# Performance work log

Measured on AMD Instinct MI355X. Metric: run time of the kernel, lower is better.

The kernel has to match this reference:

```python
import jax, jax.numpy as jnp
import numpy as np

B, C_IN, C_MID, C_OUT, R, K = 2048, 64, 64, 128, 60, 13
EPS = 1e-5


def _gather(x, nei):
    # x: [B, C, 60] -> gather neighbors -> [B, C, 60, 13]
    b, c = x.shape[0], x.shape[1]
    return x[:, :, nei].reshape(b, c, R, K)


def _block(x, nei, g, bta, m, v, W, c):
    # BN (eval mode) -> ReLU -> Conv2d(kernel (1,13)) fused block.
    h = _gather(x, nei)                              # [B,C,60,13]
    inv = g * jax.lax.rsqrt(v + EPS)                 # [C]
    h = jax.nn.relu(h * inv[None, :, None, None] + (bta - m * inv)[None, :, None, None])
    # Conv2d with kernel (1,13), stride 1 == contraction over (c, k)
    return jnp.einsum('bcrk,ock->bor', h, W) + c[None, :, None]  # [B,O,60]


def setup_inputs() -> dict:
    key = jax.random.key(0)
    ks = jax.random.split(key, 24)
    n = lambda k, s: jax.random.normal(k, s, dtype=jnp.float32)
    u = lambda k, s: jax.random.uniform(k, s, dtype=jnp.float32, minval=0.5, maxval=1.5)
    return {
        "x": n(ks[0], (B, C_IN, R)),
        "nei": jax.random.randint(ks[1], (R * K,), 0, R, dtype=jnp.int32),
        # comb_layer_in: BN(in) + Conv(in->mid)
        "g1": n(ks[2], (C_IN,)), "b1": n(ks[3], (C_IN,)), "m1": n(ks[4], (C_IN,)), "v1": u(ks[5], (C_IN,)),
        "W1": n(ks[6], (C_MID, C_IN, K)) * 0.1, "c1": n(ks[7], (C_MID,)) * 0.1,
        # comb_layer_out: BN(mid) + Conv(mid->out)
        "g2": n(ks[8], (C_MID,)), "b2": n(ks[9], (C_MID,)), "m2": n(ks[10], (C_MID,)), "v2": u(ks[11], (C_MID,)),
        "W2": n(ks[12], (C_OUT, C_MID, K)) * 0.1, "c2": n(ks[13], (C_OUT,)) * 0.1,
        # short_cut_layer: BN(in) + Conv(in->out)
        "g3": n(ks[14], (C_IN,)), "b3": n(ks[15], (C_IN,)), "m3": n(ks[16], (C_IN,)), "v3": u(ks[17], (C_IN,)),
        "W3": n(ks[18], (C_OUT, C_IN, K)) * 0.1, "c3": n(ks[19], (C_OUT,)) * 0.1,
    }


def reference(x, nei, g1, b1, m1, v1, W1, c1, g2, b2, m2, v2, W2, c2,
              g3, b3, m3, v3, W3, c3):
    f = _block(x, nei, g1, b1, m1, v1, W1, c1)      # [B, C_MID, 60]
    f = _block(f, nei, g2, b2, m2, v2, W2, c2)      # [B, C_OUT, 60]
    sc = _block(x, nei, g3, b3, m3, v3, W3, c3)     # [B, C_OUT, 60]
    return f + sc
```

## Files before the change

kernel.cpp:

```cpp
#include <hip/hip_runtime.h>
#include <hip/hip_bf16.h>


typedef __attribute__((ext_vector_type(8))) short bf16x8;
typedef __attribute__((ext_vector_type(4))) float f32x4;
typedef __attribute__((ext_vector_type(4))) unsigned short us4;
typedef __attribute__((ext_vector_type(8))) unsigned short us8;

#define EPSV 1e-5f
#define PLANE 131072
#define ZTOT  7864320

__device__ __forceinline__ unsigned short f2bf(float f) {
  unsigned int u = __builtin_bit_cast(unsigned int, f);
  u += 0x7FFFu + ((u >> 16) & 1u);
  return (unsigned short)(u >> 16);
}
__device__ __forceinline__ float bf2f(unsigned short s) {
  unsigned int u = ((unsigned int)s) << 16;
  return __builtin_bit_cast(float, u);
}

typedef const __attribute__((address_space(1))) unsigned int gas_u32;
typedef __attribute__((address_space(3))) unsigned int las_u32;
__device__ __forceinline__ void gl16(const void* g, void* l) {
  __builtin_amdgcn_global_load_lds((gas_u32*)g, (las_u32*)l, 16, 0, 0);
}

__global__ void prep_w(const float* __restrict__ W1, const float* __restrict__ W2,
                       const float* __restrict__ W3,
                       const float* __restrict__ g1, const float* __restrict__ be1,
                       const float* __restrict__ mu1, const float* __restrict__ va1,
                       const float* __restrict__ c1,
                       const float* __restrict__ g2, const float* __restrict__ be2,
                       const float* __restrict__ mu2, const float* __restrict__ va2,
                       const float* __restrict__ c2,
                       const float* __restrict__ g3, const float* __restrict__ be3,
                       const float* __restrict__ mu3, const float* __restrict__ va3,
                       const float* __restrict__ c3,
                       unsigned short* __restrict__ W1t,
                       unsigned short* __restrict__ W23t,
                       float* __restrict__ params) {
  int t = blockIdx.x * 256 + threadIdx.x;
  if (t < 4096) {
    int o = t >> 6, c = t & 63;
    const float* src = W1 + (o * 64 + c) * 13;
    unsigned short* dst = W1t + o * 832 + c;
    #pragma unroll
    for (int ks = 0; ks < 13; ks++) dst[ks * 64] = f2bf(src[ks]);
  } else if (t < 20480) {
    int idx = t - 4096;
    int half = idx >> 13;
    int o = (idx >> 6) & 127, c = idx & 63;
    const float* src = (half ? W3 : W2) + (o * 64 + c) * 13;
    unsigned short* dst = W23t + o * 1664 + half * 13 * 64 + c;
    #pragma unroll
    for (int ks = 0; ks < 13; ks++) dst[ks * 64] = f2bf(src[ks]);
  }
  if (blockIdx.x == 79) {
    int u = threadIdx.x;
    if (u < 64) {
      float a1v = g1[u] * rsqrtf(va1[u] + EPSV);
      params[u]       = a1v;
      params[64 + u]  = be1[u] - mu1[u] * a1v;
      float a3v = g3[u] * rsqrtf(va3[u] + EPSV);
      params[128 + u] = a3v;
      params[192 + u] = be3[u] - mu3[u] * a3v;
      float a2v = g2[u] * rsqrtf(va2[u] + EPSV);
      params[256 + u] = a2v;
      params[320 + u] = be2[u] - mu2[u] * a2v + a2v * c1[u];
    }
    if (u < 128) params[384 + u] = c2[u] + c3[u];
  }
}

__global__ __launch_bounds__(256) void t_in(const float* __restrict__ x,
                                            const float* __restrict__ params,
                                            unsigned short* __restrict__ z1T,
                                            unsigned short* __restrict__ z3T) {
  __shared__ float xt[64 * 61];
  __shared__ float prm[256];
  const int b = blockIdx.x, t = threadIdx.x;
  prm[t] = params[t];
  for (int i = t; i < 3840; i += 256) {
    int c = i / 60;
    xt[c * 61 + (i - c * 60)] = x[b * 3840 + i];
  }
  __syncthreads();
  if (t < 240) {
    int r = t >> 2, g = t & 3, c0 = g << 4;
    us8 z1v0, z1v1, z3v0, z3v1;
    #pragma unroll
    for (int j = 0; j < 8; j++) {
      int c = c0 + j;
      float v = xt[c * 61 + r];
      z1v0[j] = f2bf(fmaxf(fmaf(v, prm[c], prm[64 + c]), 0.f));
      z3v0[j] = f2bf(fmaxf(fmaf(v, prm[128 + c], prm[192 + c]), 0.f));
    }
    #pragma unroll
    for (int j = 0; j < 8; j++) {
      int c = c0 + 8 + j;
      float v = xt[c * 61 + r];
      z1v1[j] = f2bf(fmaxf(fmaf(v, prm[c], prm[64 + c]), 0.f));
      z3v1[j] = f2bf(fmaxf(fmaf(v, prm[128 + c], prm[192 + c]), 0.f));
    }
    int idx = (r * 2048 + b) * 64 + c0;
    *(us8*)(z1T + idx) = z1v0;  *(us8*)(z1T + idx + 8) = z1v1;
    *(us8*)(z3T + idx) = z3v0;  *(us8*)(z3T + idx + 8) = z3v1;
  }
}

#define MFMA __builtin_amdgcn_mfma_f32_16x16x32_bf16

__global__ __launch_bounds__(256, 2) void gemm1(const unsigned short* __restrict__ W1t,
                                                const unsigned short* __restrict__ z1T,
                                                const int* __restrict__ nei,
                                                const float* __restrict__ params,
                                                unsigned short* __restrict__ z2T) {
  __shared__ unsigned short As[2][4096];
  __shared__ unsigned short Bs[2][2][8192];

  const int bid = blockIdx.x;
  const int rp = bid >> 4, btile = bid & 15;
  const int b0 = btile << 7;
  const int rA = rp * 2, rB = rA + 1;
  const int t = threadIdx.x, wave = t >> 6, lane = t & 63;
  const int quad = lane >> 4, nl = lane & 15;
  const int rsel = wave >> 1, nhh = wave & 1;

  int pl0[13], pl1[13];
  #pragma unroll
  for (int q = 0; q < 13; q++) { pl0[q] = nei[rA * 13 + q]; pl1[q] = nei[rB * 13 + q]; }

  const int trow = t >> 3, tj = t & 7;
  const int sw8 = ((tj ^ (trow & 7)) << 3);
  const unsigned short* gA = W1t + trow * 832 + tj * 8;
  const unsigned short* gB = z1T + (b0 + trow) * 64 + tj * 8;
  unsigned short* lA = &As[0][trow * 64 + sw8];
  unsigned short* lB0 = &Bs[0][0][trow * 64 + sw8];
  unsigned short* lB1 = &Bs[0][1][trow * 64 + sw8];

  {
    us8 va0 = *(const us8*)(gA);
    us8 va1 = *(const us8*)(gA + 32 * 832);
    const unsigned short* g0 = gB + pl0[0] * PLANE;
    const unsigned short* g1p = gB + pl1[0] * PLANE;
    us8 b00 = *(const us8*)(g0);
    us8 b01 = *(const us8*)(g0 + 2048);
    us8 b02 = *(const us8*)(g0 + 4096);
    us8 b03 = *(const us8*)(g0 + 6144);
    us8 b10 = *(const us8*)(g1p);
    us8 b11 = *(const us8*)(g1p + 2048);
    us8 b12 = *(const us8*)(g1p + 4096);
    us8 b13 = *(const us8*)(g1p + 6144);
    *(us8*)(lA) = va0;  *(us8*)(lA + 2048) = va1;
    *(us8*)(lB0) = b00; *(us8*)(lB0 + 2048) = b01;
    *(us8*)(lB0 + 4096) = b02; *(us8*)(lB0 + 6144) = b03;
    *(us8*)(lB1) = b10; *(us8*)(lB1 + 2048) = b11;
    *(us8*)(lB1 + 4096) = b12; *(us8*)(lB1 + 6144) = b13;
  }
  __syncthreads();

  const int c0 = ((quad ^ (nl & 7)) << 3);
  f32x4 acc[4][4] = {};
  #pragma unroll 1
  for (int kq = 0; kq < 13; kq++) {
    const int bf = kq & 1;
    us8 va0, va1, b00, b01, b02, b03, b10, b11, b12, b13;
    if (kq < 12) {
      const unsigned short* ga = gA + (kq + 1) * 64;
      va0 = *(const us8*)(ga);
      va1 = *(const us8*)(ga + 32 * 832);
      const unsigned short* g0 = gB + pl0[kq + 1] * PLANE;
      const unsigned short* g1p = gB + pl1[kq + 1] * PLANE;
      b00 = *(const us8*)(g0);        b01 = *(const us8*)(g0 + 2048);
      b02 = *(const us8*)(g0 + 4096); b03 = *(const us8*)(g0 + 6144);
      b10 = *(const us8*)(g1p);        b11 = *(const us8*)(g1p + 2048);
      b12 = *(const us8*)(g1p + 4096); b13 = *(const us8*)(g1p + 6144);
    }
    const unsigned short* Ab = &As[bf][nl * 64];
    const unsigned short* Bb = &Bs[bf][rsel][(nhh * 64 + nl) * 64];
    bf16x8 af[4][2], bfr[4][2];
    #pragma unroll
    for (int mt = 0; mt < 4; mt++) {
      af[mt][0] = *(const bf16x8*)(Ab + mt * 1024 + c0);
      af[mt][1] = *(const bf16x8*)(Ab + mt * 1024 + (c0 ^ 32));
    }
    #pragma unroll
    for (int nt = 0; nt < 4; nt++) {
      bfr[nt][0] = *(const bf16x8*)(Bb + nt * 1024 + c0);
      bfr[nt][1] = *(const bf16x8*)(Bb + nt * 1024 + (c0 ^ 32));
    }
    #pragma unroll
    for (int h = 0; h < 2; h++)
      #pragma unroll
      for (int mt = 0; mt < 4; mt++)
        #pragma unroll
        for (int nt = 0; nt < 4; nt++)
          acc[mt][nt] = MFMA(af[mt][h], bfr[nt][h], acc[mt][nt], 0, 0, 0);
    if (kq < 12) {
      unsigned short* la = lA + (bf ^ 1) * 4096;
      unsigned short* l0 = lB0 + (bf ^ 1) * 16384;
      unsigned short* l1 = lB1 + (bf ^ 1) * 16384;
      *(us8*)(la) = va0;  *(us8*)(la + 2048) = va1;
      *(us8*)(l0) = b00; *(us8*)(l0 + 2048) = b01;
      *(us8*)(l0 + 4096) = b02; *(us8*)(l0 + 6144) = b03;
      *(us8*)(l1) = b10; *(us8*)(l1 + 2048) = b11;
      *(us8*)(l1 + 4096) = b12; *(us8*)(l1 + 6144) = b13;
    }
    __syncthreads();
  }

  const int rr = rA + rsel;
  #pragma unroll
  for (int mt = 0; mt < 4; mt++) {
    int ob = mt * 16 + quad * 4;
    f32x4 av = *(const f32x4*)(params + 256 + ob);
    f32x4 bv = *(const f32x4*)(params + 320 + ob);
    #pragma unroll
    for (int nt = 0; nt < 4; nt++) {
      int col = b0 + nhh * 64 + nt * 16 + nl;
      f32x4 a = acc[mt][nt];
      us4 w;
      w.x = f2bf(fmaxf(fmaf(a[0], av[0], bv[0]), 0.f));
      w.y = f2bf(fmaxf(fmaf(a[1], av[1], bv[1]), 0.f));
      w.z = f2bf(fmaxf(fmaf(a[2], av[2], bv[2]), 0.f));
      w.w = f2bf(fmaxf(fmaf(a[3], av[3], bv[3]), 0.f));
      *(us4*)(z2T + (rr * 2048 + col) * 64 + ob) = w;
    }
  }
}

__global__ __launch_bounds__(256, 2) void gemm2(const unsigned short* __restrict__ W23t,
                                                const unsigned short* __restrict__ z2T,
                                                const unsigned short* __restrict__ z3T,
                                                const int* __restrict__ nei,
                                                const float* __restrict__ params,
                                                unsigned short* __restrict__ outT) {
  __shared__ unsigned short As[2][4096];
  __shared__ unsigned short Bs[2][8192];

  const int bid = blockIdx.x;
  const int r = bid >> 3, btile = bid & 7;
  const int b0 = btile << 8;
  const int t = threadIdx.x, wv = t >> 6, lane = t & 63;
  const int quad = lane >> 4, nl = lane & 15;
  const int mh = wv >> 1, nh = wv & 1;

  const int neibase = r * 13;

  const int lr = lane >> 2, lj = lane & 3;
  int aoff[2];
  #pragma unroll
  for (int i = 0; i < 2; i++) aoff[i] = (16 * (2 * wv + i) + lr) * 3328 + lj * 16;
  int boff[4];
  #pragma unroll
  for (int i = 0; i < 4; i++) boff[i] = (b0 + 16 * (4 * wv + i) + lr) * 128 + lj * 16;

  const char* gAb = (const char*)W23t;

  {
    int p0 = nei[neibase];
    const char* gb = (const char*)(z2T + p0 * PLANE);
    #pragma unroll
    for (int i = 0; i < 2; i++)
      gl16(gAb + aoff[i], &As[0][(2 * wv + i) * 512]);
    #pragma unroll
    for (int i = 0; i < 4; i++)
      gl16(gb + boff[i], &Bs[0][(4 * wv + i) * 512]);
  }
  asm volatile("s_waitcnt vmcnt(0)" ::: "memory");
  __syncthreads();

  f32x4 acc[4][8] = {};
  #pragma unroll 1
  for (int s = 0; s < 52; s++) {
    const int buf = s & 1;
    if (s < 51) {
      const int kn = s + 1;
      const int pn = kn >> 1, hn = kn & 1;
      int p = nei[neibase + (pn < 13 ? pn : pn - 13)];
      const char* ga = gAb + pn * 128 + hn * 64;
      const char* gb = (const char*)((pn < 13 ? z2T : z3T) + p * PLANE) + hn * 64;
      #pragma unroll
      for (int i = 0; i < 2; i++)
        gl16(ga + aoff[i], &As[buf ^ 1][(2 * wv + i) * 512]);
      #pragma unroll
      for (int i = 0; i < 4; i++)
        gl16(gb + boff[i], &Bs[buf ^ 1][(4 * wv + i) * 512]);
    }
    const unsigned short* Ab = &As[buf][(mh * 64 + nl) * 32 + quad * 8];
    const unsigned short* Bb = &Bs[buf][(nh * 128 + nl) * 32 + quad * 8];
    bf16x8 af[4], bfr[8];
    #pragma unroll
    for (int mt = 0; mt < 4; mt++)
      af[mt] = *(const bf16x8*)(Ab + mt * 512);
    #pragma unroll
    for (int nt = 0; nt < 8; nt++)
      bfr[nt] = *(const bf16x8*)(Bb + nt * 512);
    #pragma unroll
    for (int mt = 0; mt < 4; mt++)
      #pragma unroll
      for (int nt = 0; nt < 8; nt++)
        acc[mt][nt] = MFMA(af[mt], bfr[nt], acc[mt][nt], 0, 0, 0);
    asm volatile("s_waitcnt vmcnt(0)" ::: "memory");
    __syncthreads();
  }

  #pragma unroll
  for (int mt = 0; mt < 4; mt++) {
    int ob = mh * 64 + mt * 16 + quad * 4;
    f32x4 cv = *(const f32x4*)(params + 384 + ob);
    #pragma unroll
    for (int nt = 0; nt < 8; nt++) {
      int col = b0 + nh * 128 + nt * 16 + nl;
      f32x4 a = acc[mt][nt];
      us4 w;
      w.x = f2bf(a[0] + cv[0]);
      w.y = f2bf(a[1] + cv[1]);
      w.z = f2bf(a[2] + cv[2]);
      w.w = f2bf(a[3] + cv[3]);
      *(us4*)(outT + (r * 2048 + col) * 128 + ob) = w;
    }
  }
}

__global__ __launch_bounds__(256) void t_out(const unsigned short* __restrict__ outT,
                                             float* __restrict__ out) {
  __shared__ float ot[60 * 129];
  const int b = blockIdx.x, t = threadIdx.x;
  for (int i = t; i < 1920; i += 256) {
    int r = i >> 5, og = (i & 31) << 2;
    us4 v = *(const us4*)(outT + (r * 2048 + b) * 128 + og);
    ot[r * 129 + og + 0] = bf2f(v.x);
    ot[r * 129 + og + 1] = bf2f(v.y);
    ot[r * 129 + og + 2] = bf2f(v.z);
    ot[r * 129 + og + 3] = bf2f(v.w);
  }
  __syncthreads();
  int o = t >> 1, s = t & 1;
  float* dst = out + b * 7680 + o * 60 + s * 30;
  #pragma unroll
  for (int j = 0; j < 30; j++) dst[j] = ot[(s * 30 + j) * 129 + o];
}

extern "C" void kernel_launch(void* const* d_in, const int* in_sizes, int n_in,
                              void* d_out, int out_size, void* d_ws, size_t ws_size,
                              hipStream_t stream) {
  const float* x   = (const float*)d_in[0];
  const int*   nei = (const int*)d_in[1];
  const float* g1  = (const float*)d_in[2];
  const float* be1 = (const float*)d_in[3];
  const float* mu1 = (const float*)d_in[4];
  const float* va1 = (const float*)d_in[5];
  const float* W1  = (const float*)d_in[6];
  const float* c1  = (const float*)d_in[7];
  const float* g2  = (const float*)d_in[8];
  const float* be2 = (const float*)d_in[9];
  const float* mu2 = (const float*)d_in[10];
  const float* va2 = (const float*)d_in[11];
  const float* W2  = (const float*)d_in[12];
  const float* c2  = (const float*)d_in[13];
  const float* g3  = (const float*)d_in[14];
  const float* be3 = (const float*)d_in[15];
  const float* mu3 = (const float*)d_in[16];
  const float* va3 = (const float*)d_in[17];
  const float* W3  = (const float*)d_in[18];
  const float* c3  = (const float*)d_in[19];

  unsigned short* W1t  = (unsigned short*)d_ws;
  unsigned short* W23t = W1t + 53248;
  float*          prm  = (float*)(W23t + 212992);
  unsigned short* z2T  = (unsigned short*)(prm + 512);
  unsigned short* z3T  = z2T + ZTOT;
  unsigned short* big  = z3T + ZTOT;
  unsigned short* z1T  = big;
  unsigned short* outT = big;

  prep_w<<<80, 256, 0, stream>>>(W1, W2, W3,
                                 g1, be1, mu1, va1, c1,
                                 g2, be2, mu2, va2, c2,
                                 g3, be3, mu3, va3, c3,
                                 W1t, W23t, prm);
  t_in<<<2048, 256, 0, stream>>>(x, prm, z1T, z3T);
  gemm1<<<480, 256, 0, stream>>>(W1t, z1T, nei, prm, z2T);
  gemm2<<<480, 256, 0, stream>>>(W23t, z2T, z3T, nei, prm, outT);
  t_out<<<2048, 256, 0, stream>>>(outT, (float*)d_out);
}
```

Baseline: 245.0 us.

## Triple-buffer gemm2 LDS loads with swizzled layout and precomputed neighbor offsets

```diff
diff --git a/kernel.cpp b/kernel.cpp
--- a/kernel.cpp
+++ b/kernel.cpp
@@ -237,8 +237,9 @@
                                                 const int* __restrict__ nei,
                                                 const float* __restrict__ params,
                                                 unsigned short* __restrict__ outT) {
-  __shared__ unsigned short As[2][4096];
-  __shared__ unsigned short Bs[2][8192];
+  __shared__ unsigned short As[3][4096];
+  __shared__ unsigned short Bs[3][8192];
+  __shared__ int sOff[26];
 
   const int bid = blockIdx.x;
   const int r = bid >> 3, btile = bid & 7;
@@ -247,50 +248,62 @@
   const int quad = lane >> 4, nl = lane & 15;
   const int mh = wv >> 1, nh = wv & 1;
 
-  const int neibase = r * 13;
+  if (t < 26) {
+    int idx = t < 13 ? t : t - 13;
+    int p = nei[r * 13 + idx];
+    sOff[t] = p * (PLANE * 2) + (t < 13 ? 0 : ZTOT * 2);
+  }
 
   const int lr = lane >> 2, lj = lane & 3;
+  const int sj = ((lj ^ ((lr >> 1) & 3)) << 4);
   int aoff[2];
   #pragma unroll
-  for (int i = 0; i < 2; i++) aoff[i] = (16 * (2 * wv + i) + lr) * 3328 + lj * 16;
+  for (int i = 0; i < 2; i++) aoff[i] = (16 * (2 * wv + i) + lr) * 3328 + sj;
   int boff[4];
   #pragma unroll
-  for (int i = 0; i < 4; i++) boff[i] = (b0 + 16 * (4 * wv + i) + lr) * 128 + lj * 16;
+  for (int i = 0; i < 4; i++) boff[i] = (b0 + 16 * (4 * wv + i) + lr) * 128 + sj;
 
   const char* gAb = (const char*)W23t;
+  const char* z2b = (const char*)z2T;
+
+  __syncthreads();
 
   {
-    int p0 = nei[neibase];
-    const char* gb = (const char*)(z2T + p0 * PLANE);
-    #pragma unroll
-    for (int i = 0; i < 2; i++)
-      gl16(gAb + aoff[i], &As[0][(2 * wv + i) * 512]);
-    #pragma unroll
-    for (int i = 0; i < 4; i++)
-      gl16(gb + boff[i], &Bs[0][(4 * wv + i) * 512]);
-  }
-  asm volatile("s_waitcnt vmcnt(0)" ::: "memory");
-  __syncthreads();
+    const char* gb = z2b + sOff[0];
+    #pragma unroll
+    for (int i = 0; i < 2; i++) gl16(gAb + aoff[i], &As[0][(2 * wv + i) * 512]);
+    #pragma unroll
+    for (int i = 0; i < 4; i++) gl16(gb + boff[i], &Bs[0][(4 * wv + i) * 512]);
+    #pragma unroll
+    for (int i = 0; i < 2; i++) gl16(gAb + 64 + aoff[i], &As[1][(2 * wv + i) * 512]);
+    #pragma unroll
+    for (int i = 0; i < 4; i++) gl16(gb + 64 + boff[i], &Bs[1][(4 * wv + i) * 512]);
+  }
+
+  const int rc = ((quad ^ ((nl >> 1) & 3)) << 3);
+  const int aro = (mh * 64 + nl) * 32 + rc;
+  const int bro = (nh * 128 + nl) * 32 + rc;
 
   f32x4 acc[4][8] = {};
+  int cb = 0, sb = 2;
   #pragma unroll 1
-  for (int s = 0; s < 52; s++) {
-    const int buf = s & 1;
-    if (s < 51) {
-      const int kn = s + 1;
-      const int pn = kn >> 1, hn = kn & 1;
-      int p = nei[neibase + (pn < 13 ? pn : pn - 13)];
-      const char* ga = gAb + pn * 128 + hn * 64;
-      const char* gb = (const char*)((pn < 13 ? z2T : z3T) + p * PLANE) + hn * 64;
+  for (int s = 0; s < 51; s++) {
+    asm volatile("s_waitcnt vmcnt(6)" ::: "memory");
+    __builtin_amdgcn_s_barrier();
+    __builtin_amdgcn_sched_barrier(0);
+    const int kn = s + 2;
+    if (kn < 52) {
+      const int pn = kn >> 1;
+      int off = sOff[pn] + ((kn & 1) << 6);
+      const char* ga = gAb + kn * 64;
+      const char* gb = z2b + off;
       #pragma unroll
-      for (int i = 0; i < 2; i++)
-        gl16(ga + aoff[i], &As[buf ^ 1][(2 * wv + i) * 512]);
+      for (int i = 0; i < 2; i++) gl16(ga + aoff[i], &As[sb][(2 * wv + i) * 512]);
       #pragma unroll
-      for (int i = 0; i < 4; i++)
-        gl16(gb + boff[i], &Bs[buf ^ 1][(4 * wv + i) * 512]);
-    }
-    const unsigned short* Ab = &As[buf][(mh * 64 + nl) * 32 + quad * 8];
-    const unsigned short* Bb = &Bs[buf][(nh * 128 + nl) * 32 + quad * 8];
+      for (int i = 0; i < 4; i++) gl16(gb + boff[i], &Bs[sb][(4 * wv + i) * 512]);
+    }
+    const unsigned short* Ab = &As[cb][aro];
+    const unsigned short* Bb = &Bs[cb][bro];
     bf16x8 af[4], bfr[8];
     #pragma unroll
     for (int mt = 0; mt < 4; mt++)
@@ -303,8 +316,27 @@
       #pragma unroll
       for (int nt = 0; nt < 8; nt++)
         acc[mt][nt] = MFMA(af[mt], bfr[nt], acc[mt][nt], 0, 0, 0);
+    cb = (cb == 2) ? 0 : cb + 1;
+    sb = (sb == 2) ? 0 : sb + 1;
+  }
+  {
     asm volatile("s_waitcnt vmcnt(0)" ::: "memory");
-    __syncthreads();
+    __builtin_amdgcn_s_barrier();
+    __builtin_amdgcn_sched_barrier(0);
+    const unsigned short* Ab = &As[0][aro];
+    const unsigned short* Bb = &Bs[0][bro];
+    bf16x8 af[4], bfr[8];
+    #pragma unroll
+    for (int mt = 0; mt < 4; mt++)
+      af[mt] = *(const bf16x8*)(Ab + mt * 512);
+    #pragma unroll
+    for (int nt = 0; nt < 8; nt++)
+      bfr[nt] = *(const bf16x8*)(Bb + nt * 512);
+    #pragma unroll
+    for (int mt = 0; mt < 4; mt++)
+      #pragma unroll
+      for (int nt = 0; nt < 8; nt++)
+        acc[mt][nt] = MFMA(af[mt], bfr[nt], acc[mt][nt], 0, 0, 0);
   }
 
   #pragma unroll
```

Result: faster. 238.3 us (-2.7%).
